# Kernel optimization log

Measured on AMD Instinct MI355X. Metric: run time of the kernel, lower is better.

## Reference

```python
import jax, jax.numpy as jnp
import numpy as np

IN_BW = 4
W_BW = 4
EPS = 1e-5


def quantize(x, bw):
    # k-bit uniform quantizer on [-1, 1 - 2^(1-bw)] with straight-through rounding
    scale = 2.0 ** (bw - 1)
    xc = jnp.clip(x, -1.0, 1.0 - 1.0 / scale)
    q = jnp.round(xc * scale) / scale
    return xc + jax.lax.stop_gradient(q - xc)


def bconv(x, w, stride):
    # BinarizeConv2d: quantize activations (in_bw) and weights (weight_bw), then conv
    return jax.lax.conv_general_dilated(
        quantize(x, IN_BW), quantize(w, W_BW),
        window_strides=stride, padding='VALID',
        dimension_numbers=('NCHW', 'OIHW', 'NCHW'))


def bn2d(x, g, b):
    mean = x.mean(axis=(0, 2, 3), keepdims=True)
    var = x.var(axis=(0, 2, 3), keepdims=True)
    return (x - mean) * jax.lax.rsqrt(var + EPS) * g.reshape(1, -1, 1, 1) + b.reshape(1, -1, 1, 1)


def bn1d(x, g, b):
    mean = x.mean(axis=0, keepdims=True)
    var = x.var(axis=0, keepdims=True)
    return (x - mean) * jax.lax.rsqrt(var + EPS) * g + b


def htanh(x):
    return jnp.clip(x, -1.0, 1.0)


def setup_inputs() -> dict:
    key = jax.random.key(0)
    ks = jax.random.split(key, 24)
    B = 8192
    d = {'x': jax.random.normal(ks[0], (B, 1, 1250, 1), dtype=jnp.float32)}
    # conv weights OIHW
    shapes = [(3, 1, 6, 1), (5, 3, 5, 1), (10, 5, 4, 1), (20, 10, 4, 1), (20, 20, 4, 1)]
    for i, s in enumerate(shapes):
        d[f'w{i+1}'] = 0.3 * jax.random.normal(ks[1 + i], s, dtype=jnp.float32)
    d['fw1'] = 0.3 * jax.random.normal(ks[6], (10, 740), dtype=jnp.float32)
    d['fw2'] = 0.3 * jax.random.normal(ks[7], (2, 10), dtype=jnp.float32)
    chans = [3, 5, 10, 20, 20, 10, 2]
    for i, c in enumerate(chans):
        d[f'g{i+1}'] = 1.0 + 0.1 * jax.random.normal(ks[8 + i], (c,), dtype=jnp.float32)
        d[f'b{i+1}'] = 0.1 * jax.random.normal(ks[15 + i], (c,), dtype=jnp.float32)
    return d


def reference(x, w1, w2, w3, w4, w5, fw1, fw2,
              g1, g2, g3, g4, g5, g6, g7,
              b1, b2, b3, b4, b5, b6, b7):
    h = htanh(bn2d(bconv(x, w1, (2, 1)), g1, b1))
    h = htanh(bn2d(bconv(h, w2, (2, 1)), g2, b2))
    h = htanh(bn2d(bconv(h, w3, (2, 1)), g3, b3))
    h = htanh(bn2d(bconv(h, w4, (2, 1)), g4, b4))
    h = htanh(bn2d(bconv(h, w5, (2, 1)), g5, b5))
    h = h.reshape(h.shape[0], -1)  # (B, 20*37*1) = (B, 740)
    # dropout is identity in eval mode
    h = htanh(bn1d(quantize(h, IN_BW) @ quantize(fw1, W_BW).T, g6, b6))
    h = bn1d(quantize(h, IN_BW) @ quantize(fw2, W_BW).T, g7, b7)
    return h
```

## Files before the change

kernel.cpp:

```cpp
#include <hip/hip_runtime.h>

#define DEV __device__ __forceinline__

DEV float qwt(float w) {
    float y = fminf(fmaxf(w, -1.0f), 0.875f);
    return rintf(y * 8.0f) * 0.125f;
}
DEV int q8i(float x, float a, float b) {
    float y = fmaf(x, a, b);
    y = fminf(fmaxf(y, -1.0f), 0.875f);
    return (int)rintf(y * 8.0f);
}
DEV float qact(float x, float a, float b) {
    float y = fmaf(x, a, b);
    y = fminf(fmaxf(y, -1.0f), 0.875f);
    return rintf(y * 8.0f) * 0.125f;
}

template<int CIN,int COUT,int K,int LIN,int LINP,int LOUT,int LOUTP,int P,int R,bool IN_FLOAT>
__global__ __launch_bounds__(256) void conv_k(
    const void* __restrict__ in_, const float* __restrict__ w,
    const float* __restrict__ tr, short* __restrict__ out,
    float* __restrict__ partial, int B, int numTiles)
{
    constexpr int KP4 = (K + 3) & ~3;
    constexpr int K4  = K & ~3;
    constexpr int KR  = K - K4;
    constexpr int NV  = K + 2 * (P - 1);
    constexpr int LO_P = (LOUT + P - 1) / P;
    constexpr int GROUPS = R * LO_P;

    __shared__ __align__(16) signed char smem[R * CIN * LINP + 16];
    __shared__ __align__(16) float wq[COUT * CIN * KP4];
    __shared__ float ts[CIN], tb[CIN];
    __shared__ float red[4][2 * COUT];

    const int tid = threadIdx.x;

    for (int i = tid; i < COUT * CIN * KP4; i += 256) {
        int k = i % KP4; int ck = i / KP4;
        int ci = ck % CIN; int co = ck / CIN;
        wq[i] = (k < K) ? qwt(w[(co * CIN + ci) * K + k]) * 0.125f : 0.0f;
    }
    if constexpr (!IN_FLOAT) {
        if (tid < CIN) {
            ts[tid] = tr[tid] * 0.015625f;
            tb[tid] = tr[CIN + tid];
        }
    }

    float tsum[COUT], tsq[COUT];
#pragma unroll
    for (int c = 0; c < COUT; c++) { tsum[c] = 0.f; tsq[c] = 0.f; }

    for (int tile = blockIdx.x; tile < numTiles; tile += gridDim.x) {
        const int r0   = tile * R;
        const int rcnt = min(R, B - r0);
        __syncthreads();

        if constexpr (IN_FLOAT) {
            constexpr int CH = LIN / 2;
            const float2* gp = (const float2*)in_;
            for (int c = tid; c < rcnt * CH; c += 256) {
                int r = c / CH, rem = c - r * CH;
                float2 v = gp[(size_t)(r0 + r) * CH + rem];
                int b0 = q8i(v.x, 1.f, 0.f) & 0xff;
                int b1 = q8i(v.y, 1.f, 0.f) & 0xff;
                *(unsigned short*)(smem + r * LINP + rem * 2) =
                    (unsigned short)(b0 | (b1 << 8));
            }
        } else {
            constexpr int CH  = CIN * LINP / 8;
            constexpr int CHC = LINP / 8;
            const int4* gp = (const int4*)((const short*)in_ + (size_t)r0 * CIN * LINP);
            for (int c = tid; c < rcnt * CH; c += 256) {
                int r = c / CH, rem = c - r * CH;
                int ci = rem / CHC;
                float a = ts[ci], bo = tb[ci];
                int4 v = gp[c];
                int vs[4] = { v.x, v.y, v.z, v.w };
                unsigned pk[2];
#pragma unroll
                for (int u = 0; u < 2; u++) {
                    unsigned pp = 0;
#pragma unroll
                    for (int j = 0; j < 2; j++) {
                        int word = vs[u * 2 + j];
                        int b0 = q8i((float)(short)(word & 0xffff), a, bo) & 0xff;
                        int b1 = q8i((float)(short)(word >> 16),    a, bo) & 0xff;
                        pp |= (unsigned)(b0 | (b1 << 8)) << (16 * j);
                    }
                    pk[u] = pp;
                }
                ((uint2*)smem)[c] = make_uint2(pk[0], pk[1]);
            }
        }
        __syncthreads();

#pragma unroll 1
        for (int g = tid; g < GROUPS; g += 256) {
            int r = g / LO_P;
            if (r >= rcnt) continue;
            int l0   = (g - r * LO_P) * P;
            int pact = min(P, LOUT - l0);

            float acc[COUT][P];
#pragma unroll
            for (int co = 0; co < COUT; co++)
#pragma unroll
                for (int p = 0; p < P; p++) acc[co][p] = 0.f;

            const int ibase = r * CIN * LINP + 2 * l0;
#pragma unroll 1
            for (int ci = 0; ci < CIN; ci++) {
                float vv[NV];
#pragma unroll
                for (int j = 0; j < NV; j++)
                    vv[j] = (float)smem[ibase + ci * LINP + j];
#pragma unroll
                for (int co = 0; co < COUT; co++) {
                    const float* wrow = &wq[(co * CIN + ci) * KP4];
#pragma unroll
                    for (int c4 = 0; c4 < K4 / 4; c4++) {
                        float4 wv = *(const float4*)(wrow + 4 * c4);
#pragma unroll
                        for (int p = 0; p < P; p++) {
                            acc[co][p] = fmaf(vv[2*p + 4*c4 + 0], wv.x, acc[co][p]);
                            acc[co][p] = fmaf(vv[2*p + 4*c4 + 1], wv.y, acc[co][p]);
                            acc[co][p] = fmaf(vv[2*p + 4*c4 + 2], wv.z, acc[co][p]);
                            acc[co][p] = fmaf(vv[2*p + 4*c4 + 3], wv.w, acc[co][p]);
                        }
                    }
#pragma unroll
                    for (int u = 0; u < KR; u++) {
                        float wsc = wrow[K4 + u];
#pragma unroll
                        for (int p = 0; p < P; p++)
                            acc[co][p] = fmaf(vv[2*p + K4 + u], wsc, acc[co][p]);
                    }
                }
            }

            const size_t ob = (size_t)(r0 + r) * COUT * LOUTP + l0;
#pragma unroll
            for (int co = 0; co < COUT; co++) {
                if (pact == P) {
                    short tmp[P];
#pragma unroll
                    for (int p = 0; p < P; p++) {
                        float v = acc[co][p];
                        tmp[p] = (short)__float2int_rn(v * 64.0f);
                        tsum[co] += v;
                        tsq[co]   = fmaf(v, v, tsq[co]);
                    }
                    short* op = &out[ob + (size_t)co * LOUTP];
                    if constexpr (P == 2) {
                        *(short2*)op = make_short2(tmp[0], tmp[1]);
                    } else if constexpr (P == 4) {
                        *(short4*)op = make_short4(tmp[0], tmp[1], tmp[2], tmp[3]);
                    } else if constexpr (P == 8) {
                        *(short4*)op       = make_short4(tmp[0], tmp[1], tmp[2], tmp[3]);
                        *(short4*)(op + 4) = make_short4(tmp[4], tmp[5], tmp[6], tmp[7]);
                    } else {
#pragma unroll
                        for (int p = 0; p < P; p++) op[p] = tmp[p];
                    }
                } else {
#pragma unroll
                    for (int p = 0; p < P; p++) {
                        if (p < pact) {
                            float v = acc[co][p];
                            out[ob + (size_t)co * LOUTP + p] = (short)__float2int_rn(v * 64.0f);
                            tsum[co] += v;
                            tsq[co]   = fmaf(v, v, tsq[co]);
                        }
                    }
                }
            }
        }
    }

    const int lane = tid & 63, wid = tid >> 6;
#pragma unroll
    for (int co = 0; co < COUT; co++) {
        float s = tsum[co], q = tsq[co];
        for (int off = 32; off > 0; off >>= 1) {
            s += __shfl_down(s, off, 64);
            q += __shfl_down(q, off, 64);
        }
        if (lane == 0) { red[wid][2 * co] = s; red[wid][2 * co + 1] = q; }
    }
    __syncthreads();
    if (tid < 2 * COUT) {
        float v = red[0][tid] + red[1][tid] + red[2][tid] + red[3][tid];
        partial[(size_t)blockIdx.x * (2 * COUT) + tid] = v;
    }
}

__global__ __launch_bounds__(256) void finalize_k(
    const float* __restrict__ partial, int G, int C, double N,
    const float* __restrict__ gamma, const float* __restrict__ beta,
    float* __restrict__ trout)
{
    const int c = blockIdx.x;
    double s = 0.0, q = 0.0;
    for (int g = threadIdx.x; g < G; g += 256) {
        s += (double)partial[(size_t)g * 2 * C + 2 * c];
        q += (double)partial[(size_t)g * 2 * C + 2 * c + 1];
    }
    for (int off = 32; off > 0; off >>= 1) {
        s += __shfl_down(s, off, 64);
        q += __shfl_down(q, off, 64);
    }
    __shared__ double rs[4], rq[4];
    int lane = threadIdx.x & 63, wid = threadIdx.x >> 6;
    if (lane == 0) { rs[wid] = s; rq[wid] = q; }
    __syncthreads();
    if (threadIdx.x == 0) {
        double S = rs[0] + rs[1] + rs[2] + rs[3];
        double Q = rq[0] + rq[1] + rq[2] + rq[3];
        double mean = S / N;
        double var  = Q / N - mean * mean;
        double inv  = 1.0 / sqrt(var + 1e-5);
        double sc   = (double)gamma[c] * inv;
        trout[c]     = (float)sc;
        trout[C + c] = (float)((double)beta[c] - mean * sc);
    }
}

__global__ __launch_bounds__(256) void fc1_k(
    const short* __restrict__ y5, const float* __restrict__ fw1,
    const float* __restrict__ tr, float* __restrict__ z1,
    float* __restrict__ partial, int B)
{
    __shared__ float wq[7400];
    __shared__ float ts[20], tb[20];
    __shared__ float red[4][20];
    const int tid = threadIdx.x;
    for (int i = tid; i < 7400; i += 256) wq[i] = qwt(fw1[i]);
    if (tid < 20) { ts[tid] = tr[tid]; tb[tid] = tr[20 + tid]; }
    __syncthreads();

    const int lane = tid & 63, wid = tid >> 6;
    float tsum[10], tsq[10];
#pragma unroll
    for (int j = 0; j < 10; j++) { tsum[j] = 0.f; tsq[j] = 0.f; }

#pragma unroll 1
    for (int r = blockIdx.x * 4 + wid; r < B; r += gridDim.x * 4) {
        const short* xr = y5 + (size_t)r * 800;
        float acc[10];
#pragma unroll
        for (int j = 0; j < 10; j++) acc[j] = 0.f;
#pragma unroll 1
        for (int f = lane; f < 740; f += 64) {
            int c = f / 37, pos = f - c * 37;
            float x = qact((float)xr[c * 40 + pos] * 0.015625f, ts[c], tb[c]);
#pragma unroll
            for (int j = 0; j < 10; j++) acc[j] = fmaf(x, wq[j * 740 + f], acc[j]);
        }
#pragma unroll
        for (int j = 0; j < 10; j++) {
            float v = acc[j];
            for (int off = 1; off < 64; off <<= 1) v += __shfl_xor(v, off, 64);
            tsum[j] += v; tsq[j] = fmaf(v, v, tsq[j]);
            if (lane == j) z1[(size_t)r * 10 + j] = v;
        }
    }
    if (lane == 0) {
#pragma unroll
        for (int j = 0; j < 10; j++) { red[wid][2 * j] = tsum[j]; red[wid][2 * j + 1] = tsq[j]; }
    }
    __syncthreads();
    if (tid < 20) {
        float v = red[0][tid] + red[1][tid] + red[2][tid] + red[3][tid];
        partial[(size_t)blockIdx.x * 20 + tid] = v;
    }
}

__global__ __launch_bounds__(256) void fc2_k(
    const float* __restrict__ z1, const float* __restrict__ fw2,
    const float* __restrict__ tr, float* __restrict__ z2,
    float* __restrict__ partial, int B)
{
    __shared__ float wq[20], ts[10], tb[10];
    __shared__ float red[4][4];
    const int tid = threadIdx.x;
    if (tid < 20) wq[tid] = qwt(fw2[tid]);
    if (tid < 10) { ts[tid] = tr[tid]; tb[tid] = tr[10 + tid]; }
    __syncthreads();

    float s0 = 0.f, q0 = 0.f, s1 = 0.f, q1 = 0.f;
    const int r = blockIdx.x * 256 + tid;
    if (r < B) {
        float a0 = 0.f, a1 = 0.f;
#pragma unroll
        for (int i = 0; i < 10; i++) {
            float x = qact(z1[(size_t)r * 10 + i], ts[i], tb[i]);
            a0 = fmaf(x, wq[i], a0);
            a1 = fmaf(x, wq[10 + i], a1);
        }
        z2[(size_t)r * 2]     = a0;
        z2[(size_t)r * 2 + 1] = a1;
        s0 = a0; q0 = a0 * a0; s1 = a1; q1 = a1 * a1;
    }
    const int lane = tid & 63, wid = tid >> 6;
    for (int off = 32; off > 0; off >>= 1) {
        s0 += __shfl_down(s0, off, 64); q0 += __shfl_down(q0, off, 64);
        s1 += __shfl_down(s1, off, 64); q1 += __shfl_down(q1, off, 64);
    }
    if (lane == 0) { red[wid][0] = s0; red[wid][1] = q0; red[wid][2] = s1; red[wid][3] = q1; }
    __syncthreads();
    if (tid < 4) {
        float v = red[0][tid] + red[1][tid] + red[2][tid] + red[3][tid];
        partial[(size_t)blockIdx.x * 4 + tid] = v;
    }
}

__global__ __launch_bounds__(256) void apply_k(
    const float* __restrict__ z2, const float* __restrict__ tr,
    float* __restrict__ out, int n)
{
    int i = blockIdx.x * 256 + threadIdx.x;
    if (i < n) {
        int c = i & 1;
        out[i] = fmaf(z2[i], tr[c], tr[2 + c]);
    }
}

extern "C" void kernel_launch(void* const* d_in, const int* in_sizes, int n_in,
                              void* d_out, int out_size, void* d_ws, size_t ws_size,
                              hipStream_t stream)
{
    const float* x   = (const float*)d_in[0];
    const float* w1  = (const float*)d_in[1];
    const float* w2  = (const float*)d_in[2];
    const float* w3  = (const float*)d_in[3];
    const float* w4  = (const float*)d_in[4];
    const float* w5  = (const float*)d_in[5];
    const float* fw1 = (const float*)d_in[6];
    const float* fw2 = (const float*)d_in[7];
    const float *g[7], *bb[7];
    for (int i = 0; i < 7; i++) { g[i] = (const float*)d_in[8 + 2 * i]; bb[i] = (const float*)d_in[9 + 2 * i]; }

    char* ws = (char*)d_ws;
    size_t off = 0;
    auto alloc = [&](size_t bytes) -> void* {
        void* p = ws + off;
        off += (bytes + 255) & ~(size_t)255;
        return p;
    };
    short* SA      = (short*)alloc((size_t)8192 * 3 * 624 * 2);
    short* SB      = (short*)alloc((size_t)8192 * 20 * 80 * 2);
    float* z1      = (float*)alloc((size_t)81920 * 4);
    float* z2      = (float*)alloc((size_t)16384 * 4);
    float* partial = (float*)alloc((size_t)81920 * 4);
    float* tr2 = (float*)alloc(256); float* tr3 = (float*)alloc(256);
    float* tr4 = (float*)alloc(256); float* tr5 = (float*)alloc(256);
    float* tr6 = (float*)alloc(256); float* tr7 = (float*)alloc(256);
    float* tr8 = (float*)alloc(256);

    const int B = 8192;

    {
        int nt = (B + 7) / 8;
        conv_k<1, 3, 6, 1250, 1252, 623, 624, 8, 8, true>
            <<<nt, 256, 0, stream>>>(x, w1, nullptr, SA, partial, B, nt);
        finalize_k<<<3, 256, 0, stream>>>(partial, nt, 3, (double)B * 623.0, g[0], bb[0], tr2);
    }
    {
        int nt = (B + 7) / 8;
        conv_k<3, 5, 5, 623, 624, 310, 312, 4, 8, false>
            <<<nt, 256, 0, stream>>>(SA, w2, tr2, SB, partial, B, nt);
        finalize_k<<<5, 256, 0, stream>>>(partial, nt, 5, (double)B * 310.0, g[1], bb[1], tr3);
    }
    {
        int nt = (B + 6) / 7;
        conv_k<5, 10, 4, 310, 312, 154, 160, 4, 7, false>
            <<<nt, 256, 0, stream>>>(SB, w3, tr3, SA, partial, B, nt);
        finalize_k<<<10, 256, 0, stream>>>(partial, nt, 10, (double)B * 154.0, g[2], bb[2], tr4);
    }
    {
        int nt = (B + 12) / 13;
        conv_k<10, 20, 4, 154, 160, 76, 80, 4, 13, false>
            <<<nt, 256, 0, stream>>>(SA, w4, tr4, SB, partial, B, nt);
        finalize_k<<<20, 256, 0, stream>>>(partial, nt, 20, (double)B * 76.0, g[3], bb[3], tr5);
    }
    {
        int nt = (B + 12) / 13;
        conv_k<20, 20, 4, 76, 80, 37, 40, 2, 13, false>
            <<<nt, 256, 0, stream>>>(SB, w5, tr5, SA, partial, B, nt);
        finalize_k<<<20, 256, 0, stream>>>(partial, nt, 20, (double)B * 37.0, g[4], bb[4], tr6);
    }
    {
        int grid = 512;
        fc1_k<<<grid, 256, 0, stream>>>(SA, fw1, tr6, z1, partial, B);
        finalize_k<<<10, 256, 0, stream>>>(partial, grid, 10, (double)B, g[5], bb[5], tr7);
    }
    {
        int grid = 32;
        fc2_k<<<grid, 256, 0, stream>>>(z1, fw2, tr7, z2, partial, B);
        finalize_k<<<2, 256, 0, stream>>>(partial, grid, 2, (double)B, g[6], bb[6], tr8);
    }
    apply_k<<<64, 256, 0, stream>>>(z2, tr8, (float*)d_out, out_size);
}
```

Before: 320.5 us.

## Use int8 sdot4 convolutions with prepacked weights and fuse FC2 tail

Convolution layers now accumulate in integer arithmetic using packed int8 dot4 instructions. A single-block kernel pre-quantizes and packs the weights, and byte-aligned activation windows are extracted with alignbit. The persistent tile loop is dropped in favour of one tile per block, and the P/R tile sizes are changed per layer. The final finalize, fc2, finalize and apply kernels are merged into a single-block kernel with the whole output staged in shared memory. This cuts FP FMA count and launch overhead, at the cost of a serial one-block tail and more global weight loads in the inner loop.

```diff
diff --git a/kernel.cpp b/kernel.cpp
--- a/kernel.cpp
+++ b/kernel.cpp
@@ -5,6 +5,10 @@
 DEV float qwt(float w) {
     float y = fminf(fmaxf(w, -1.0f), 0.875f);
     return rintf(y * 8.0f) * 0.125f;
+}
+DEV int qw8i(float w) {
+    float y = fminf(fmaxf(w, -1.0f), 0.875f);
+    return (int)rintf(y * 8.0f);
 }
 DEV int q8i(float x, float a, float b) {
     float y = fmaf(x, a, b);
@@ -17,163 +21,192 @@
     return rintf(y * 8.0f) * 0.125f;
 }
 
-template<int CIN,int COUT,int K,int LIN,int LINP,int LOUT,int LOUTP,int P,int R,bool IN_FLOAT>
+DEV int dot4(int a, int b, int c) {
+#if __has_builtin(__builtin_amdgcn_sdot4)
+    return __builtin_amdgcn_sdot4(a, b, c, false);
+#else
+    c += (int)(signed char)(a)       * (int)(signed char)(b);
+    c += (int)(signed char)(a >> 8)  * (int)(signed char)(b >> 8);
+    c += (int)(signed char)(a >> 16) * (int)(signed char)(b >> 16);
+    c += (int)(signed char)(a >> 24) * (int)(signed char)(b >> 24);
+    return c;
+#endif
+}
+DEV unsigned alignpair(unsigned hi, unsigned lo, int bits) {
+#if __has_builtin(__builtin_amdgcn_alignbit)
+    return __builtin_amdgcn_alignbit(hi, lo, bits);
+#else
+    return bits ? ((lo >> bits) | (hi << (32 - bits))) : lo;
+#endif
+}
+
+DEV void pack_layer(const float* w, int* o, int CIN, int COUT, int K, int t) {
+    int KW = (K + 3) / 4;
+    for (int i = t; i < COUT * CIN * KW; i += 256) {
+        int j = i % KW, cc = i / KW;
+        unsigned r = 0;
+        for (int u = 0; u < 4; u++) {
+            int k = 4 * j + u;
+            int b = (k < K) ? (qw8i(w[cc * K + k]) & 0xff) : 0;
+            r |= (unsigned)b << (8 * u);
+        }
+        o[i] = (int)r;
+    }
+}
+__global__ __launch_bounds__(256) void pack_k(
+    const float* w1, const float* w2, const float* w3, const float* w4, const float* w5,
+    int* o1, int* o2, int* o3, int* o4, int* o5)
+{
+    int t = threadIdx.x;
+    pack_layer(w1, o1, 1, 3, 6, t);
+    pack_layer(w2, o2, 3, 5, 5, t);
+    pack_layer(w3, o3, 5, 10, 4, t);
+    pack_layer(w4, o4, 10, 20, 4, t);
+    pack_layer(w5, o5, 20, 20, 4, t);
+}
+
+template<int CIN,int COUT,int K,int LINP,int LOUT,int LOUTP,int P,int R,bool IN_FLOAT,int LIN=0>
 __global__ __launch_bounds__(256) void conv_k(
-    const void* __restrict__ in_, const float* __restrict__ w,
+    const void* __restrict__ in_, const int* __restrict__ wqi,
     const float* __restrict__ tr, short* __restrict__ out,
-    float* __restrict__ partial, int B, int numTiles)
-{
-    constexpr int KP4 = (K + 3) & ~3;
-    constexpr int K4  = K & ~3;
-    constexpr int KR  = K - K4;
-    constexpr int NV  = K + 2 * (P - 1);
+    float* __restrict__ partial, int B)
+{
+    constexpr int KW   = (K + 3) / 4;
+    constexpr int NE   = P + 2 * KW - 2 + 1;
+    constexpr int ND   = (2 * (NE - 1) + 3) / 4 + 2;
     constexpr int LO_P = (LOUT + P - 1) / P;
     constexpr int GROUPS = R * LO_P;
 
-    __shared__ __align__(16) signed char smem[R * CIN * LINP + 16];
-    __shared__ __align__(16) float wq[COUT * CIN * KP4];
-    __shared__ float ts[CIN], tb[CIN];
+    __shared__ __align__(16) signed char smem[R * CIN * LINP + 32];
+    __shared__ float ts[CIN > 0 ? CIN : 1], tb[CIN > 0 ? CIN : 1];
     __shared__ float red[4][2 * COUT];
 
     const int tid = threadIdx.x;
 
-    for (int i = tid; i < COUT * CIN * KP4; i += 256) {
-        int k = i % KP4; int ck = i / KP4;
-        int ci = ck % CIN; int co = ck / CIN;
-        wq[i] = (k < K) ? qwt(w[(co * CIN + ci) * K + k]) * 0.125f : 0.0f;
-    }
     if constexpr (!IN_FLOAT) {
         if (tid < CIN) {
             ts[tid] = tr[tid] * 0.015625f;
             tb[tid] = tr[CIN + tid];
         }
-    }
+        __syncthreads();
+    }
+
+    const int r0   = blockIdx.x * R;
+    const int rcnt = min(R, B - r0);
+
+    if constexpr (IN_FLOAT) {
+        constexpr int CH = LIN / 2;
+        const float2* gp = (const float2*)in_;
+        for (int c = tid; c < rcnt * CH; c += 256) {
+            int r = c / CH, rem = c - r * CH;
+            float2 v = gp[(size_t)(r0 + r) * CH + rem];
+            int b0 = q8i(v.x, 1.f, 0.f) & 0xff;
+            int b1 = q8i(v.y, 1.f, 0.f) & 0xff;
+            *(unsigned short*)(smem + r * LINP + rem * 2) =
+                (unsigned short)(b0 | (b1 << 8));
+        }
+    } else {
+        constexpr int CH  = CIN * LINP / 8;
+        constexpr int CHC = LINP / 8;
+        const int4* gp = (const int4*)((const short*)in_ + (size_t)r0 * CIN * LINP);
+        for (int c = tid; c < rcnt * CH; c += 256) {
+            int rem = c % CH;
+            int ci = rem / CHC;
+            float a = ts[ci], bo = tb[ci];
+            int4 v = gp[c];
+            int vs[4] = { v.x, v.y, v.z, v.w };
+            unsigned pk[2];
+#pragma unroll
+            for (int u = 0; u < 2; u++) {
+                unsigned pp = 0;
+#pragma unroll
+                for (int j = 0; j < 2; j++) {
+                    int word = vs[u * 2 + j];
+                    int b0 = q8i((float)(short)(word & 0xffff), a, bo) & 0xff;
+                    int b1 = q8i((float)(short)(word >> 16),    a, bo) & 0xff;
+                    pp |= (unsigned)(b0 | (b1 << 8)) << (16 * j);
+                }
+                pk[u] = pp;
+            }
+            ((uint2*)smem)[c] = make_uint2(pk[0], pk[1]);
+        }
+    }
+    __syncthreads();
 
     float tsum[COUT], tsq[COUT];
 #pragma unroll
     for (int c = 0; c < COUT; c++) { tsum[c] = 0.f; tsq[c] = 0.f; }
 
-    for (int tile = blockIdx.x; tile < numTiles; tile += gridDim.x) {
-        const int r0   = tile * R;
-        const int rcnt = min(R, B - r0);
-        __syncthreads();
-
-        if constexpr (IN_FLOAT) {
-            constexpr int CH = LIN / 2;
-            const float2* gp = (const float2*)in_;
-            for (int c = tid; c < rcnt * CH; c += 256) {
-                int r = c / CH, rem = c - r * CH;
-                float2 v = gp[(size_t)(r0 + r) * CH + rem];
-                int b0 = q8i(v.x, 1.f, 0.f) & 0xff;
-                int b1 = q8i(v.y, 1.f, 0.f) & 0xff;
-                *(unsigned short*)(smem + r * LINP + rem * 2) =
-                    (unsigned short)(b0 | (b1 << 8));
+#pragma unroll 1
+    for (int g = tid; g < GROUPS; g += 256) {
+        int r = g / LO_P;
+        if (r >= rcnt) continue;
+        int l0   = (g - r * LO_P) * P;
+        int pact = min(P, LOUT - l0);
+
+        int acc[COUT][P];
+#pragma unroll
+        for (int co = 0; co < COUT; co++)
+#pragma unroll
+            for (int p = 0; p < P; p++) acc[co][p] = 0;
+
+        const int ibase = r * CIN * LINP + 2 * l0;
+        const int sh    = (P % 2 == 0) ? 0 : (ibase & 3);
+
+        for (int ci = 0; ci < CIN; ci++) {
+            const int* sp = (const int*)smem + ((ci * LINP + (ibase & ~3)) >> 2);
+            int d[ND];
+#pragma unroll
+            for (int j = 0; j < ND; j++) d[j] = sp[j];
+            int e[NE];
+#pragma unroll
+            for (int i = 0; i < NE; i++) {
+                int off = sh + 2 * i;
+                e[i] = (int)alignpair((unsigned)d[off / 4 + 1], (unsigned)d[off / 4], (off & 3) * 8);
             }
-        } else {
-            constexpr int CH  = CIN * LINP / 8;
-            constexpr int CHC = LINP / 8;
-            const int4* gp = (const int4*)((const short*)in_ + (size_t)r0 * CIN * LINP);
-            for (int c = tid; c < rcnt * CH; c += 256) {
-                int r = c / CH, rem = c - r * CH;
-                int ci = rem / CHC;
-                float a = ts[ci], bo = tb[ci];
-                int4 v = gp[c];
-                int vs[4] = { v.x, v.y, v.z, v.w };
-                unsigned pk[2];
-#pragma unroll
-                for (int u = 0; u < 2; u++) {
-                    unsigned pp = 0;
-#pragma unroll
-                    for (int j = 0; j < 2; j++) {
-                        int word = vs[u * 2 + j];
-                        int b0 = q8i((float)(short)(word & 0xffff), a, bo) & 0xff;
-                        int b1 = q8i((float)(short)(word >> 16),    a, bo) & 0xff;
-                        pp |= (unsigned)(b0 | (b1 << 8)) << (16 * j);
-                    }
-                    pk[u] = pp;
-                }
-                ((uint2*)smem)[c] = make_uint2(pk[0], pk[1]);
-            }
-        }
-        __syncthreads();
-
-#pragma unroll 1
-        for (int g = tid; g < GROUPS; g += 256) {
-            int r = g / LO_P;
-            if (r >= rcnt) continue;
-            int l0   = (g - r * LO_P) * P;
-            int pact = min(P, LOUT - l0);
-
-            float acc[COUT][P];
-#pragma unroll
-            for (int co = 0; co < COUT; co++)
-#pragma unroll
-                for (int p = 0; p < P; p++) acc[co][p] = 0.f;
-
-            const int ibase = r * CIN * LINP + 2 * l0;
-#pragma unroll 1
-            for (int ci = 0; ci < CIN; ci++) {
-                float vv[NV];
-#pragma unroll
-                for (int j = 0; j < NV; j++)
-                    vv[j] = (float)smem[ibase + ci * LINP + j];
-#pragma unroll
-                for (int co = 0; co < COUT; co++) {
-                    const float* wrow = &wq[(co * CIN + ci) * KP4];
-#pragma unroll
-                    for (int c4 = 0; c4 < K4 / 4; c4++) {
-                        float4 wv = *(const float4*)(wrow + 4 * c4);
-#pragma unroll
-                        for (int p = 0; p < P; p++) {
-                            acc[co][p] = fmaf(vv[2*p + 4*c4 + 0], wv.x, acc[co][p]);
-                            acc[co][p] = fmaf(vv[2*p + 4*c4 + 1], wv.y, acc[co][p]);
-                            acc[co][p] = fmaf(vv[2*p + 4*c4 + 2], wv.z, acc[co][p]);
-                            acc[co][p] = fmaf(vv[2*p + 4*c4 + 3], wv.w, acc[co][p]);
-                        }
-                    }
-#pragma unroll
-                    for (int u = 0; u < KR; u++) {
-                        float wsc = wrow[K4 + u];
-#pragma unroll
-                        for (int p = 0; p < P; p++)
-                            acc[co][p] = fmaf(vv[2*p + K4 + u], wsc, acc[co][p]);
-                    }
+#pragma unroll
+            for (int co = 0; co < COUT; co++) {
+#pragma unroll
+                for (int j = 0; j < KW; j++) {
+                    int wv = wqi[(co * CIN + ci) * KW + j];
+#pragma unroll
+                    for (int p = 0; p < P; p++)
+                        acc[co][p] = dot4(e[p + 2 * j], wv, acc[co][p]);
                 }
             }
-
-            const size_t ob = (size_t)(r0 + r) * COUT * LOUTP + l0;
-#pragma unroll
-            for (int co = 0; co < COUT; co++) {
-                if (pact == P) {
-                    short tmp[P];
-#pragma unroll
-                    for (int p = 0; p < P; p++) {
-                        float v = acc[co][p];
-                        tmp[p] = (short)__float2int_rn(v * 64.0f);
+        }
+
+        const size_t ob = (size_t)(r0 + r) * COUT * LOUTP + l0;
+#pragma unroll
+        for (int co = 0; co < COUT; co++) {
+            if (pact == P) {
+                short tmp[P];
+#pragma unroll
+                for (int p = 0; p < P; p++) {
+                    tmp[p] = (short)acc[co][p];
+                    float v = (float)acc[co][p] * 0.015625f;
+                    tsum[co] += v;
+                    tsq[co]   = fmaf(v, v, tsq[co]);
+                }
+                short* op = &out[ob + (size_t)co * LOUTP];
+                if constexpr (P == 1) {
+                    op[0] = tmp[0];
+                } else if constexpr (P == 2) {
+                    *(short2*)op = make_short2(tmp[0], tmp[1]);
+                } else if constexpr (P == 4) {
+                    *(short4*)op = make_short4(tmp[0], tmp[1], tmp[2], tmp[3]);
+                } else if constexpr (P == 8) {
+                    *(short4*)op       = make_short4(tmp[0], tmp[1], tmp[2], tmp[3]);
+                    *(short4*)(op + 4) = make_short4(tmp[4], tmp[5], tmp[6], tmp[7]);
+                }
+            } else {
+#pragma unroll
+                for (int p = 0; p < P; p++) {
+                    if (p < pact) {
+                        out[ob + (size_t)co * LOUTP + p] = (short)acc[co][p];
+                        float v = (float)acc[co][p] * 0.015625f;
                         tsum[co] += v;
                         tsq[co]   = fmaf(v, v, tsq[co]);
-                    }
-                    short* op = &out[ob + (size_t)co * LOUTP];
-                    if constexpr (P == 2) {
-                        *(short2*)op = make_short2(tmp[0], tmp[1]);
-                    } else if constexpr (P == 4) {
-                        *(short4*)op = make_short4(tmp[0], tmp[1], tmp[2], tmp[3]);
-                    } else if constexpr (P == 8) {
-                        *(short4*)op       = make_short4(tmp[0], tmp[1], tmp[2], tmp[3]);
-                        *(short4*)(op + 4) = make_short4(tmp[4], tmp[5], tmp[6], tmp[7]);
-                    } else {
-#pragma unroll
-                        for (int p = 0; p < P; p++) op[p] = tmp[p];
-                    }
-                } else {
-#pragma unroll
-                    for (int p = 0; p < P; p++) {
-                        if (p < pact) {
-                            float v = acc[co][p];
-                            out[ob + (size_t)co * LOUTP + p] = (short)__float2int_rn(v * 64.0f);
-                            tsum[co] += v;
-                            tsq[co]   = fmaf(v, v, tsq[co]);
-                        }
                     }
                 }
             }
@@ -278,53 +311,87 @@
     }
 }
 
-__global__ __launch_bounds__(256) void fc2_k(
+__global__ __launch_bounds__(256) void fc2_fused_k(
     const float* __restrict__ z1, const float* __restrict__ fw2,
-    const float* __restrict__ tr, float* __restrict__ z2,
-    float* __restrict__ partial, int B)
-{
-    __shared__ float wq[20], ts[10], tb[10];
-    __shared__ float red[4][4];
+    const float* __restrict__ part6, int G6,
+    const float* __restrict__ g6, const float* __restrict__ b6,
+    const float* __restrict__ g7, const float* __restrict__ b7,
+    float* __restrict__ outp, int B)
+{
+    __shared__ float zbuf[16384];
+    __shared__ double dred[4][20];
+    __shared__ double dtot[20];
+    __shared__ float ts7[10], tb7[10], wq2[20];
+    __shared__ float fr[4][4];
+    __shared__ float tr8[4];
+
     const int tid = threadIdx.x;
-    if (tid < 20) wq[tid] = qwt(fw2[tid]);
-    if (tid < 10) { ts[tid] = tr[tid]; tb[tid] = tr[10 + tid]; }
+    const int lane = tid & 63, wid = tid >> 6;
+
+    double ls[20];
+#pragma unroll
+    for (int c = 0; c < 20; c++) ls[c] = 0.0;
+    for (int g = tid; g < G6; g += 256) {
+#pragma unroll
+        for (int c = 0; c < 20; c++) ls[c] += (double)part6[(size_t)g * 20 + c];
+    }
+#pragma unroll
+    for (int c = 0; c < 20; c++) {
+        double v = ls[c];
+        for (int off = 32; off > 0; off >>= 1) v += __shfl_down(v, off, 64);
+        if (lane == 0) dred[wid][c] = v;
+    }
+    if (tid < 20) wq2[tid] = qwt(fw2[tid]);
+    __syncthreads();
+    if (tid < 20) dtot[tid] = dred[0][tid] + dred[1][tid] + dred[2][tid] + dred[3][tid];
+    __syncthreads();
+    if (tid < 10) {
+        double N = (double)B;
+        double mean = dtot[2 * tid] / N;
+        double var  = dtot[2 * tid + 1] / N - mean * mean;
+        double inv  = 1.0 / sqrt(var + 1e-5);
+        double sc   = (double)g6[tid] * inv;
+        ts7[tid] = (float)sc;
+        tb7[tid] = (float)((double)b6[tid] - mean * sc);
+    }
     __syncthreads();
 
     float s0 = 0.f, q0 = 0.f, s1 = 0.f, q1 = 0.f;
-    const int r = blockIdx.x * 256 + tid;
-    if (r < B) {
+#pragma unroll 1
+    for (int r = tid; r < B; r += 256) {
         float a0 = 0.f, a1 = 0.f;
 #pragma unroll
         for (int i = 0; i < 10; i++) {
-            float x = qact(z1[(size_t)r * 10 + i], ts[i], tb[i]);
-            a0 = fmaf(x, wq[i], a0);
-            a1 = fmaf(x, wq[10 + i], a1);
-        }
-        z2[(size_t)r * 2]     = a0;
-        z2[(size_t)r * 2 + 1] = a1;
-        s0 = a0; q0 = a0 * a0; s1 = a1; q1 = a1 * a1;
-    }
-    const int lane = tid & 63, wid = tid >> 6;
+            float x = qact(z1[(size_t)r * 10 + i], ts7[i], tb7[i]);
+            a0 = fmaf(x, wq2[i], a0);
+            a1 = fmaf(x, wq2[10 + i], a1);
+        }
+        zbuf[r * 2]     = a0;
+        zbuf[r * 2 + 1] = a1;
+        s0 += a0; q0 = fmaf(a0, a0, q0);
+        s1 += a1; q1 = fmaf(a1, a1, q1);
+    }
     for (int off = 32; off > 0; off >>= 1) {
         s0 += __shfl_down(s0, off, 64); q0 += __shfl_down(q0, off, 64);
         s1 += __shfl_down(s1, off, 64); q1 += __shfl_down(q1, off, 64);
     }
-    if (lane == 0) { red[wid][0] = s0; red[wid][1] = q0; red[wid][2] = s1; red[wid][3] = q1; }
-    __syncthreads();
-    if (tid < 4) {
-        float v = red[0][tid] + red[1][tid] + red[2][tid] + red[3][tid];
-        partial[(size_t)blockIdx.x * 4 + tid] = v;
-    }
-}
-
-__global__ __launch_bounds__(256) void apply_k(
-    const float* __restrict__ z2, const float* __restrict__ tr,
-    float* __restrict__ out, int n)
-{
-    int i = blockIdx.x * 256 + threadIdx.x;
-    if (i < n) {
+    if (lane == 0) { fr[wid][0] = s0; fr[wid][1] = q0; fr[wid][2] = s1; fr[wid][3] = q1; }
+    __syncthreads();
+    if (tid < 2) {
+        double S = 0.0, Q = 0.0;
+        for (int w = 0; w < 4; w++) { S += (double)fr[w][2 * tid]; Q += (double)fr[w][2 * tid + 1]; }
+        double N = (double)B;
+        double mean = S / N;
+        double var  = Q / N - mean * mean;
+        double inv  = 1.0 / sqrt(var + 1e-5);
+        double sc   = (double)g7[tid] * inv;
+        tr8[tid]     = (float)sc;
+        tr8[2 + tid] = (float)((double)b7[tid] - mean * sc);
+    }
+    __syncthreads();
+    for (int i = tid; i < 2 * B; i += 256) {
         int c = i & 1;
-        out[i] = fmaf(z2[i], tr[c], tr[2 + c]);
+        outp[i] = fmaf(zbuf[i], tr8[c], tr8[2 + c]);
     }
 }
 
@@ -353,54 +420,53 @@
     short* SA      = (short*)alloc((size_t)8192 * 3 * 624 * 2);
     short* SB      = (short*)alloc((size_t)8192 * 20 * 80 * 2);
     float* z1      = (float*)alloc((size_t)81920 * 4);
-    float* z2      = (float*)alloc((size_t)16384 * 4);
     float* partial = (float*)alloc((size_t)81920 * 4);
+    int*   wp1 = (int*)alloc(64);   int* wp2 = (int*)alloc(256);
+    int*   wp3 = (int*)alloc(256);  int* wp4 = (int*)alloc(1024);
+    int*   wp5 = (int*)alloc(2048);
     float* tr2 = (float*)alloc(256); float* tr3 = (float*)alloc(256);
     float* tr4 = (float*)alloc(256); float* tr5 = (float*)alloc(256);
-    float* tr6 = (float*)alloc(256); float* tr7 = (float*)alloc(256);
-    float* tr8 = (float*)alloc(256);
+    float* tr6 = (float*)alloc(256);
 
     const int B = 8192;
 
-    {
-        int nt = (B + 7) / 8;
-        conv_k<1, 3, 6, 1250, 1252, 623, 624, 8, 8, true>
-            <<<nt, 256, 0, stream>>>(x, w1, nullptr, SA, partial, B, nt);
-        finalize_k<<<3, 256, 0, stream>>>(partial, nt, 3, (double)B * 623.0, g[0], bb[0], tr2);
-    }
-    {
-        int nt = (B + 7) / 8;
-        conv_k<3, 5, 5, 623, 624, 310, 312, 4, 8, false>
-            <<<nt, 256, 0, stream>>>(SA, w2, tr2, SB, partial, B, nt);
-        finalize_k<<<5, 256, 0, stream>>>(partial, nt, 5, (double)B * 310.0, g[1], bb[1], tr3);
-    }
-    {
-        int nt = (B + 6) / 7;
-        conv_k<5, 10, 4, 310, 312, 154, 160, 4, 7, false>
-            <<<nt, 256, 0, stream>>>(SB, w3, tr3, SA, partial, B, nt);
-        finalize_k<<<10, 256, 0, stream>>>(partial, nt, 10, (double)B * 154.0, g[2], bb[2], tr4);
-    }
-    {
-        int nt = (B + 12) / 13;
-        conv_k<10, 20, 4, 154, 160, 76, 80, 4, 13, false>
-            <<<nt, 256, 0, stream>>>(SA, w4, tr4, SB, partial, B, nt);
-        finalize_k<<<20, 256, 0, stream>>>(partial, nt, 20, (double)B * 76.0, g[3], bb[3], tr5);
-    }
-    {
-        int nt = (B + 12) / 13;
-        conv_k<20, 20, 4, 76, 80, 37, 40, 2, 13, false>
-            <<<nt, 256, 0, stream>>>(SB, w5, tr5, SA, partial, B, nt);
-        finalize_k<<<20, 256, 0, stream>>>(partial, nt, 20, (double)B * 37.0, g[4], bb[4], tr6);
+    pack_k<<<1, 256, 0, stream>>>(w1, w2, w3, w4, w5, wp1, wp2, wp3, wp4, wp5);
+
+    {
+        int grid = (B + 2) / 3;
+        conv_k<1, 3, 6, 1252, 623, 624, 8, 3, true, 1250>
+            <<<grid, 256, 0, stream>>>(x, wp1, nullptr, SA, partial, B);
+        finalize_k<<<3, 256, 0, stream>>>(partial, grid, 3, (double)B * 623.0, g[0], bb[0], tr2);
+    }
+    {
+        int grid = (B + 5) / 6;
+        conv_k<3, 5, 5, 624, 310, 312, 8, 6, false>
+            <<<grid, 256, 0, stream>>>(SA, wp2, tr2, SB, partial, B);
+        finalize_k<<<5, 256, 0, stream>>>(partial, grid, 5, (double)B * 310.0, g[1], bb[1], tr3);
+    }
+    {
+        int grid = (B + 5) / 6;
+        conv_k<5, 10, 4, 312, 154, 160, 4, 6, false>
+            <<<grid, 256, 0, stream>>>(SB, wp3, tr3, SA, partial, B);
+        finalize_k<<<10, 256, 0, stream>>>(partial, grid, 10, (double)B * 154.0, g[2], bb[2], tr4);
+    }
+    {
+        int grid = (B + 6) / 7;
+        conv_k<10, 20, 4, 160, 76, 80, 2, 7, false>
+            <<<grid, 256, 0, stream>>>(SA, wp4, tr4, SB, partial, B);
+        finalize_k<<<20, 256, 0, stream>>>(partial, grid, 20, (double)B * 76.0, g[3], bb[3], tr5);
+    }
+    {
+        int grid = (B + 6) / 7;
+        conv_k<20, 20, 4, 80, 37, 40, 1, 7, false>
+            <<<grid, 256, 0, stream>>>(SB, wp5, tr5, SA, partial, B);
+        finalize_k<<<20, 256, 0, stream>>>(partial, grid, 20, (double)B * 37.0, g[4], bb[4], tr6);
     }
     {
         int grid = 512;
         fc1_k<<<grid, 256, 0, stream>>>(SA, fw1, tr6, z1, partial, B);
-        finalize_k<<<10, 256, 0, stream>>>(partial, grid, 10, (double)B, g[5], bb[5], tr7);
-    }
-    {
-        int grid = 32;
-        fc2_k<<<grid, 256, 0, stream>>>(z1, fw2, tr7, z2, partial, B);
-        finalize_k<<<2, 256, 0, stream>>>(partial, grid, 2, (double)B, g[6], bb[6], tr8);
-    }
-    apply_k<<<64, 256, 0, stream>>>(z2, tr8, (float*)d_out, out_size);
-}
+    }
+    fc2_fused_k<<<1, 256, 0, stream>>>(z1, fw2, partial, 512,
+                                       g[5], bb[5], g[6], bb[6],
+                                       (float*)d_out, B);
+}
```

New measurement: 305.8 us. 4.6% less time.
